# Kernel tuning notes

Hardware: AMD Instinct MI355X
Metric: run time of the kernel (lower is better)

The kernel has to match this reference:

```python
import jax, jax.numpy as jnp
import numpy as np

NUM_CLASSES = 81
OUTPUT_SIZE = 19
NMS_THRESH = 0.45
TOP_K = 400          # pre-NMS candidates per class == max_output_size of tf NMS
KEEP_TOP_K = 200
CONF_THRESH = 0.01
MASK_CONF_THRESH = 0.6
B = 8
P = 24564


def setup_inputs() -> dict:
    key = jax.random.key(0)
    k1, k2, k3, k4 = jax.random.split(key, 4)
    # structured x = [loc | conf | priorbox | variances] so the decode math is realistic
    loc = 0.1 * jax.random.normal(k1, (B, P, 4), dtype=jnp.float32)
    conf = jax.random.uniform(k2, (B, P, NUM_CLASSES), dtype=jnp.float32)
    cxcy = jax.random.uniform(k3, (P, 2), minval=0.05, maxval=0.95)
    wh = jax.random.uniform(k4, (P, 2), minval=0.05, maxval=0.3)
    pmin = jnp.clip(cxcy - 0.5 * wh, 0.0, 1.0)
    pmax = jnp.clip(cxcy + 0.5 * wh, 0.0, 1.0)
    priors = jnp.broadcast_to(jnp.concatenate([pmin, pmax], -1), (B, P, 4)).astype(jnp.float32)
    variances = jnp.full((B, P, 4), 0.1, dtype=jnp.float32)
    x = jnp.concatenate([loc, conf, priors, variances], -1)
    return {"x": x}


def decode_boxes(loc, prior, var):
    pw = prior[..., 2] - prior[..., 0]
    ph = prior[..., 3] - prior[..., 1]
    pcx = 0.5 * (prior[..., 2] + prior[..., 0])
    pcy = 0.5 * (prior[..., 3] + prior[..., 1])
    cx = loc[..., 0] * pw * var[..., 0] + pcx
    cy = loc[..., 1] * pw * var[..., 1] + pcy  # uses prior_width, faithful to original code
    w = jnp.exp(loc[..., 2] * var[..., 2]) * pw
    h = jnp.exp(loc[..., 3] * var[..., 3]) * ph
    box = jnp.stack([cx - 0.5 * w, cy - 0.5 * h, cx + 0.5 * w, cy + 0.5 * h], -1)
    return jnp.clip(box, 0.0, 1.0)


def iou_matrix(b):  # [N,4] xyxy -> [N,N]
    area = (b[:, 2] - b[:, 0]) * (b[:, 3] - b[:, 1])
    ix1 = jnp.maximum(b[:, None, 0], b[None, :, 0])
    iy1 = jnp.maximum(b[:, None, 1], b[None, :, 1])
    ix2 = jnp.minimum(b[:, None, 2], b[None, :, 2])
    iy2 = jnp.minimum(b[:, None, 3], b[None, :, 3])
    inter = jnp.maximum(ix2 - ix1, 0.0) * jnp.maximum(iy2 - iy1, 0.0)
    union = area[:, None] + area[None, :] - inter
    return jnp.where(union > 0.0, inter / union, 0.0)


def greedy_nms(iou, valid):  # candidates already sorted desc by score
    n = valid.shape[0]
    def body(kept, i):
        sup = jnp.any(kept & (iou[i] > NMS_THRESH))
        return kept.at[i].set(valid[i] & ~sup), None
    kept, _ = jax.lax.scan(body, jnp.zeros(n, dtype=bool), jnp.arange(n))
    return kept


def _forward(x):
    b = x.shape[0]
    loc = x[..., :4]
    conf = x[..., 4:4 + NUM_CLASSES]
    prior = x[..., -8:-4]
    var = x[..., -4:]
    boxes = decode_boxes(loc, prior, var)                        # [B,P,4]
    cls_conf = jnp.swapaxes(conf[..., 1:], 1, 2)                 # [B,C-1,P] (skip background class 0)
    masked = jnp.where(cls_conf > CONF_THRESH, cls_conf, -1.0)
    scores, idx = jax.lax.top_k(masked, TOP_K)                   # [B,C-1,K]
    cand = jnp.take_along_axis(boxes[:, None], idx[..., None], axis=2)  # [B,C-1,K,4]
    valid = scores > CONF_THRESH
    iou = jax.vmap(jax.vmap(iou_matrix))(cand)                   # [B,C-1,K,K]
    kept = jax.vmap(jax.vmap(greedy_nms))(iou, valid)            # [B,C-1,K]
    labels = jnp.broadcast_to(jnp.arange(1, NUM_CLASSES)[None, :, None], scores.shape)
    det_scores = jnp.where(kept, scores, -1.0).reshape(b, -1)
    det_boxes = cand.reshape(b, -1, 4)
    det_labels = labels.reshape(b, -1)
    order = jnp.argsort(-det_scores, axis=1)[:, :KEEP_TOP_K]     # sort desc by conf, keep_top_k=200
    top_s = jnp.take_along_axis(det_scores, order, 1)            # [B,200]
    top_b = jnp.take_along_axis(det_boxes, order[..., None], 1)  # [B,200,4]
    top_l = jnp.take_along_axis(det_labels, order, 1)            # [B,200]

    def rasterize(s, bx, lb):
        vld = s >= MASK_CONF_THRESH
        co = jnp.round(bx * OUTPUT_SIZE).astype(jnp.int32)       # [K,4] x1,y1,x2,y2
        g = jnp.arange(OUTPUT_SIZE)
        cover = ((g[None, :, None] >= co[:, 1, None, None]) & (g[None, :, None] < co[:, 3, None, None]) &
                 (g[None, None, :] >= co[:, 0, None, None]) & (g[None, None, :] < co[:, 2, None, None]) &
                 vld[:, None, None])                             # [K,S,S]
        chan = lb - 1                                            # label-1 channel, as in original
        kidx = jnp.arange(KEEP_TOP_K)
        def per_channel(c):
            cov = cover & (chan == c)[:, None, None]
            win = jnp.max(jnp.where(cov, kidx[:, None, None], -1), axis=0)  # [S,S]
            return jnp.where(win >= 0, s[jnp.clip(win, 0)], 0.0)
        return jnp.transpose(jax.vmap(per_channel)(jnp.arange(NUM_CLASSES)), (1, 2, 0))

    return jax.vmap(rasterize)(top_s, top_b, top_l)              # [B,S,S,C]


def reference(x):
    return _forward(x)
```

## Files before the change

### kernel.cpp

```cpp
#include <hip/hip_runtime.h>

#define NB 8
#define NP 24564
#define NCLS 80
#define TOPK 400
#define KEEPK 200
#define OUTS 19
#define NCELL (OUTS * OUTS)
#define DETN (NCLS * TOPK)
#define CKS 32008
#define ROWS 128
#define CHUNKS ((NP + ROWS - 1) / ROWS)
#define CAP 1024
#define T0 0.972f
#define NT 512
#define LCAP 24
#define CSTR 16
#define SUBS 8
#define SUBCAP 128
#define WTASK 2704
#define TILN 676
#define SKW(i) ((unsigned)(i) + ((unsigned)(i) >> 5))
#define SELN (TOPK + (TOPK >> 5) + 4)

__device__ __forceinline__ unsigned f2ord(float f) {
    unsigned u = __float_as_uint(f);
    return (u & 0x80000000u) ? ~u : (u | 0x80000000u);
}
__device__ __forceinline__ float ord2f(unsigned k) {
    unsigned u = (k & 0x80000000u) ? (k & 0x7fffffffu) : ~k;
    return __uint_as_float(u);
}
__device__ __forceinline__ unsigned bin16(unsigned key) {
    int b = (int)(key >> 16) - 0xBC00;
    b = b < 0 ? 0 : (b > 1023 ? 1023 : b);
    return (unsigned)b;
}

__device__ __forceinline__ unsigned long long shfl_xor_u64(unsigned long long v, int mask) {
    unsigned lo = (unsigned)__shfl_xor((int)(unsigned)v, mask);
    unsigned hi = (unsigned)__shfl_xor((int)(v >> 32), mask);
    return ((unsigned long long)hi << 32) | lo;
}

__device__ __forceinline__ void regsort1024(unsigned long long& a0, unsigned long long& a1,
                                            unsigned long long* sc, unsigned t) {
    const unsigned e0 = 2u * t;
#pragma unroll
    for (unsigned k = 2; k <= 1024; k <<= 1) {
#pragma unroll
        for (unsigned j = k >> 1; j >= 128; j >>= 1) {
            sc[e0] = a0; sc[e0 + 1] = a1;
            __syncthreads();
            unsigned p0 = e0 ^ j;
            unsigned long long b0 = sc[p0], b1 = sc[p0 + 1];
            bool km = ((e0 & k) == 0u) ^ ((e0 & j) != 0u);
            a0 = km ? (a0 > b0 ? a0 : b0) : (a0 < b0 ? a0 : b0);
            a1 = km ? (a1 > b1 ? a1 : b1) : (a1 < b1 ? a1 : b1);
            __syncthreads();
        }
#pragma unroll
        for (unsigned j = ((k >> 1) < 64u ? (k >> 1) : 64u); j >= 2; j >>= 1) {
            unsigned long long b0 = shfl_xor_u64(a0, (int)(j >> 1));
            unsigned long long b1 = shfl_xor_u64(a1, (int)(j >> 1));
            bool km = ((e0 & k) == 0u) ^ ((e0 & j) != 0u);
            a0 = km ? (a0 > b0 ? a0 : b0) : (a0 < b0 ? a0 : b0);
            a1 = km ? (a1 > b1 ? a1 : b1) : (a1 < b1 ? a1 : b1);
        }
        {
            bool dir = ((e0 & k) == 0u);
            unsigned long long mx = a0 > a1 ? a0 : a1;
            unsigned long long mn = a0 > a1 ? a1 : a0;
            a0 = dir ? mx : mn;
            a1 = dir ? mn : mx;
        }
    }
}

__device__ __forceinline__ void bitonic_desc(unsigned long long* cand, unsigned S, int tid) {
    for (unsigned k = 2; k <= S; k <<= 1)
        for (unsigned j = k >> 1; j; j >>= 1) {
            for (unsigned i = tid; i < S; i += NT) {
                unsigned l = i ^ j;
                if (l > i) {
                    unsigned long long a = cand[i], bq = cand[l];
                    bool sw = ((i & k) == 0) ? (a < bq) : (a > bq);
                    if (sw) { cand[i] = bq; cand[l] = a; }
                }
            }
            __syncthreads();
        }
}

__global__ __launch_bounds__(256) void kZ(unsigned* __restrict__ ccnt,
                                          unsigned* __restrict__ gflag,
                                          unsigned* __restrict__ kcnt) {
    int t = blockIdx.x * 256 + threadIdx.x;
    for (int i = t; i < NB * NCLS * SUBS * CSTR; i += gridDim.x * 256) ccnt[i] = 0u;
    if (t < NB * NCLS) gflag[t] = 0u;
    if (t < NB * 16) kcnt[t] = 0u;
}

__global__ __launch_bounds__(NT) void kA(const float* __restrict__ x,
                                         float4* __restrict__ boxes,
                                         unsigned long long* __restrict__ pcand,
                                         unsigned* __restrict__ ccnt,
                                         unsigned* __restrict__ gflag) {
    __shared__ float tile[ROWS * 93];
    __shared__ unsigned long long list[NCLS * LCAP];
    __shared__ unsigned lcnt[NCLS];
    __shared__ unsigned lbase[NCLS];

    int blk = blockIdx.x;
    int b = blk / CHUNKS, chunk = blk % CHUNKS;
    unsigned sub = (unsigned)(chunk & (SUBS - 1));
    int p0 = chunk * ROWS;
    int nrows = NP - p0; if (nrows > ROWS) nrows = ROWS;
    const float* src = x + (size_t)(b * NP + p0) * 93;
    int total4 = (nrows * 93) >> 2;
    const float4* s4 = (const float4*)src;
    float4* t4 = (float4*)tile;
    for (int e = threadIdx.x; e < total4; e += NT) t4[e] = s4[e];
    __syncthreads();

    int lane = threadIdx.x & 63;
    int cg = threadIdx.x >> 6;
    for (int c = cg; c < NCLS; c += (NT / 64)) {
        unsigned cnt = 0u;
        for (int h = 0; h < 2; ++h) {
            int row = h * 64 + lane;
            float v = (row < nrows) ? tile[row * 93 + 5 + c] : -1.0f;
            bool pred = v > T0;
            unsigned long long bal = __ballot(pred);
            if (pred) {
                unsigned r = cnt + (unsigned)__popcll(bal & ((1ull << lane) - 1ull));
                if (r < LCAP)
                    list[c * LCAP + r] =
                        ((unsigned long long)f2ord(v) << 32) |
                        (unsigned)(~(unsigned)(p0 + row));
            }
            cnt += (unsigned)__popcll(bal);
        }
        if (lane == 0) lcnt[c] = cnt;
    }
    __syncthreads();

    if (threadIdx.x >= 128 && threadIdx.x < 128 + NCLS) {
        int c = threadIdx.x - 128;
        unsigned n = lcnt[c];
        unsigned wr = (n > LCAP) ? LCAP : n;
        unsigned old = 0u;
        if (wr) old = atomicAdd(&ccnt[((b * NCLS + c) * SUBS + sub) * CSTR], wr);
        lbase[c] = old;
        lcnt[c] = wr;
        if (n > LCAP || old + wr > SUBCAP) gflag[b * NCLS + c] = 1u;
    }
    if (threadIdx.x < nrows) {
        const float* r = tile + threadIdx.x * 93;
        float l0 = r[0], l1 = r[1], l2 = r[2], l3 = r[3];
        float px1 = r[85], py1 = r[86], px2 = r[87], py2 = r[88];
        float v0 = r[89], v1 = r[90], v2 = r[91], v3 = r[92];
        float pw = px2 - px1, ph = py2 - py1;
        float pcx = 0.5f * (px2 + px1), pcy = 0.5f * (py2 + py1);
        float cx = l0 * pw * v0 + pcx;
        float cy = l1 * pw * v1 + pcy;
        float w = expf(l2 * v2) * pw;
        float h = expf(l3 * v3) * ph;
        float x1 = fminf(fmaxf(cx - 0.5f * w, 0.f), 1.f);
        float y1 = fminf(fmaxf(cy - 0.5f * h, 0.f), 1.f);
        float x2 = fminf(fmaxf(cx + 0.5f * w, 0.f), 1.f);
        float y2 = fminf(fmaxf(cy + 0.5f * h, 0.f), 1.f);
        boxes[(size_t)b * NP + p0 + threadIdx.x] = make_float4(x1, y1, x2, y2);
    }
    __syncthreads();

    for (int idx = threadIdx.x; idx < NCLS * LCAP; idx += NT) {
        int c = idx / LCAP, i = idx - c * LCAP;
        if ((unsigned)i < lcnt[c]) {
            unsigned pos = lbase[c] + (unsigned)i;
            if (pos < SUBCAP)
                pcand[((size_t)(b * NCLS + c) << 10) + sub * SUBCAP + pos] = list[idx];
        }
    }
}

__device__ void select_strided(const float* __restrict__ src, unsigned needed,
                               unsigned long long* cand,
                               unsigned* hist, unsigned* aux, unsigned* scal,
                               int tid) {
    for (int i = tid; i < 1024; i += NT) hist[i] = 0u;
    if (tid == 0) { scal[0] = 0u; scal[1] = 0u; scal[2] = 0u; scal[3] = 0u; }
    __syncthreads();
    for (int p = tid; p < NP; p += NT) {
        float v = src[(size_t)p * 93];
        float m = (v > 0.01f) ? v : -1.0f;
        atomicAdd(&hist[bin16(f2ord(m))], 1u);
    }
    __syncthreads();
    unsigned h0 = 0, h1 = 0, h2 = 0, h3 = 0;
    if (tid < 256) {
        h0 = hist[4 * tid]; h1 = hist[4 * tid + 1];
        h2 = hist[4 * tid + 2]; h3 = hist[4 * tid + 3];
        aux[tid] = h0 + h1 + h2 + h3;
    }
    __syncthreads();
    for (int d = 1; d < 256; d <<= 1) {
        unsigned v = 0u;
        if (tid < 256 && tid + d < 256) v = aux[tid + d];
        __syncthreads();
        if (tid < 256) aux[tid] += v;
        __syncthreads();
    }
    if (tid < 256) {
        unsigned above = (tid < 255) ? aux[tid + 1] : 0u;
        unsigned s3 = above + h3, s2 = s3 + h2, s1 = s2 + h1, s0 = s1 + h0;
        if (s0 >= needed && s1 < needed) { scal[0] = 4 * tid;     scal[1] = s1;    scal[2] = s0; }
        if (s1 >= needed && s2 < needed) { scal[0] = 4 * tid + 1; scal[1] = s2;    scal[2] = s1; }
        if (s2 >= needed && s3 < needed) { scal[0] = 4 * tid + 2; scal[1] = s3;    scal[2] = s2; }
        if (s3 >= needed && above < needed) { scal[0] = 4 * tid + 3; scal[1] = above; scal[2] = s3; }
    }
    __syncthreads();
    unsigned cb = scal[0], countHigh = scal[1], countAt = scal[2];
    unsigned cut8 = 0;
    if (countAt > CAP) {
        if (tid < 256) aux[tid] = 0u;
        __syncthreads();
        for (int p = tid; p < NP; p += NT) {
            float v = src[(size_t)p * 93];
            float m = (v > 0.01f) ? v : -1.0f;
            unsigned k = f2ord(m);
            if (bin16(k) == cb) atomicAdd(&aux[(k >> 8) & 255u], 1u);
        }
        __syncthreads();
        for (int d = 1; d < 256; d <<= 1) {
            unsigned v = 0u;
            if (tid < 256 && tid + d < 256) v = aux[tid + d];
            __syncthreads();
            if (tid < 256) aux[tid] += v;
            __syncthreads();
        }
        if (tid < 256) {
            unsigned suf8 = aux[tid];
            unsigned sufN = (tid < 255) ? aux[tid + 1] : 0u;
            unsigned need2 = needed - countHigh;
            if (suf8 >= need2 && sufN < need2) scal[3] = (unsigned)tid;
        }
        __syncthreads();
        cut8 = scal[3];
    }
    __syncthreads();
    if (tid == 0) scal[1] = 0u;
    __syncthreads();
    for (int p = tid; p < NP; p += NT) {
        float v = src[(size_t)p * 93];
        float m = (v > 0.01f) ? v : -1.0f;
        unsigned key = f2ord(m);
        unsigned b16 = bin16(key);
        bool take = (b16 > cb) || (b16 == cb && ((key >> 8) & 255u) >= cut8);
        if (take) {
            unsigned pos = atomicAdd(&scal[1], 1u);
            if (pos < CAP) cand[pos] = ((unsigned long long)key << 32) | (unsigned)(~p);
        }
    }
    __syncthreads();
    unsigned cc = scal[1]; if (cc > CAP) cc = CAP;
    for (unsigned i = tid; i < CAP; i += NT) if (i >= cc) cand[i] = 0ull;
    __syncthreads();
    bitonic_desc(cand, (cc <= 512u) ? 512u : (unsigned)CAP, tid);
}

union ScratchU {
    unsigned long long sc[1024];
    unsigned iouRowP[WTASK];
    struct { unsigned long long cand[CAP]; unsigned hist[1024]; unsigned aux[256]; } fb;
};

__global__ __launch_bounds__(NT) void kNms(const float* __restrict__ x,
                                           const float4* __restrict__ boxes,
                                           const unsigned long long* __restrict__ pcand,
                                           const unsigned* __restrict__ ccnt,
                                           const unsigned* __restrict__ gflag,
                                           unsigned long long* __restrict__ ckeys,
                                           float4* __restrict__ cboxesC,
                                           unsigned* __restrict__ kcnt) {
    __shared__ ScratchU U;
    __shared__ float4 selBox[SELN];
    __shared__ float selArea[SELN];
    __shared__ unsigned selKey[SELN];
    __shared__ unsigned short taskGW[TILN];
    __shared__ unsigned csub[SUBS];
    __shared__ unsigned scal[4];
    __shared__ unsigned Vsh;
    __shared__ unsigned keptWords[13];

    int b = blockIdx.x / NCLS, c = blockIdx.x % NCLS;
    int tid = threadIdx.x;
    unsigned t = (unsigned)tid;

    if (tid == 0) Vsh = 0u;
    if (tid < 100) {
        unsigned g = t, v = g >> 3, r = g & 7u;
        unsigned O = g + 4u * v * (v - 1u) + r * v;
        for (unsigned w = 0; w <= v; ++w)
            taskGW[O + w] = (unsigned short)((g << 4) | w);
    }
    if (tid < SUBS) {
        unsigned v = ccnt[((b * NCLS + c) * SUBS + t) * CSTR];
        csub[t] = (v > SUBCAP) ? (unsigned)SUBCAP : v;
    }
    unsigned gf = gflag[b * NCLS + c];
    __syncthreads();
    unsigned total = csub[0] + csub[1] + csub[2] + csub[3]
                   + csub[4] + csub[5] + csub[6] + csub[7];

    bool fast = (gf == 0u) && (total >= TOPK);
    unsigned long long a0, a1;
    if (fast) {
        const ulonglong2* src2 =
            (const ulonglong2*)(pcand + ((size_t)(b * NCLS + c) << 10));
        ulonglong2 vv = src2[t];
        unsigned s = t >> 6;
        unsigned o0 = (2u * t) & (SUBCAP - 1u);
        unsigned cs = csub[s];
        a0 = (o0     < cs) ? vv.x : 0ull;
        a1 = (o0 + 1 < cs) ? vv.y : 0ull;
        regsort1024(a0, a1, U.sc, t);
    } else {
        select_strided(x + (size_t)b * NP * 93 + 5 + c, TOPK,
                       U.fb.cand, U.fb.hist, U.fb.aux, scal, tid);
        a0 = U.fb.cand[2u * t];
        a1 = U.fb.cand[2u * t + 1];
    }
    const unsigned VALID_KEY = f2ord(0.01f);
    if (t < TOPK / 2) {
        unsigned i0 = ~(unsigned)a0; if (i0 >= NP) i0 = 0;
        unsigned i1 = ~(unsigned)a1; if (i1 >= NP) i1 = 0;
        float4 b0 = boxes[(size_t)b * NP + i0];
        float4 b1 = boxes[(size_t)b * NP + i1];
        selBox[SKW(2u * t)] = b0;            selBox[SKW(2u * t + 1)] = b1;
        selArea[SKW(2u * t)] = (b0.z - b0.x) * (b0.w - b0.y);
        selArea[SKW(2u * t + 1)] = (b1.z - b1.x) * (b1.w - b1.y);
        selKey[SKW(2u * t)] = (unsigned)(a0 >> 32);
        selKey[SKW(2u * t + 1)] = (unsigned)(a1 >> 32);
    }
    {
        bool v0 = (t < TOPK / 2) && ((unsigned)(a0 >> 32) > VALID_KEY);
        bool v1 = (t < TOPK / 2) && ((unsigned)(a1 >> 32) > VALID_KEY);
        unsigned long long bv0 = __ballot(v0), bv1 = __ballot(v1);
        if ((t & 63u) == 0u)
            atomicAdd(&Vsh, (unsigned)(__popcll(bv0) + __popcll(bv1)));
    }
    __syncthreads();

    for (int T = tid; T < TILN; T += NT) {
        unsigned gw = (unsigned)taskGW[T];
        unsigned g = gw >> 4, w = gw & 15u;
        unsigned r0 = 4u * g;
        float4 br0 = selBox[SKW(r0)];     float ar0 = selArea[SKW(r0)];
        float4 br1 = selBox[SKW(r0 + 1)]; float ar1 = selArea[SKW(r0 + 1)];
        float4 br2 = selBox[SKW(r0 + 2)]; float ar2 = selArea[SKW(r0 + 2)];
        float4 br3 = selBox[SKW(r0 + 3)]; float ar3 = selArea[SKW(r0 + 3)];
        unsigned w0 = 0, w1 = 0, w2 = 0, w3 = 0;
#pragma unroll 8
        for (int jj = 0; jj < 32; ++jj) {
            int j = (int)(w * 32u) + jj;
            float4 bj = selBox[SKW(j)];
            float aj = selArea[SKW(j)];
#define IOU1(BR, AR, WRD) { \
            float ix = fminf(BR.z, bj.z) - fmaxf(BR.x, bj.x); \
            float iy = fminf(BR.w, bj.w) - fmaxf(BR.y, bj.y); \
            float inter = fmaxf(ix, 0.f) * fmaxf(iy, 0.f); \
            float uni = AR + aj - inter; \
            WRD |= (unsigned)(inter > 0.45f * uni) << jj; }
            IOU1(br0, ar0, w0) IOU1(br1, ar1, w1)
            IOU1(br2, ar2, w2) IOU1(br3, ar3, w3)
#undef IOU1
        }
        unsigned band = g >> 3;
        unsigned baseo = (band + 1u) * (16u * band + (r0 & 31u)) + w;
        U.iouRowP[baseo]                   = w0;
        U.iouRowP[baseo +      (band + 1u)] = w1;
        U.iouRowP[baseo + 2u * (band + 1u)] = w2;
        U.iouRowP[baseo + 3u * (band + 1u)] = w3;
    }
    __syncthreads();

    if (tid < 64) {
        unsigned lane = t;
        unsigned myKept = 0;
        unsigned V = Vsh;
        unsigned q0 = U.iouRowP[0 + lane], q1 = U.iouRowP[1 + lane];
        unsigned q2 = U.iouRowP[2 + lane], q3 = U.iouRowP[3 + lane];
        unsigned q4 = U.iouRowP[4 + lane], q5 = U.iouRowP[5 + lane];
        unsigned q6 = U.iouRowP[6 + lane], q7 = U.iouRowP[7 + lane];
#define STEP(Q, II) { \
        unsigned w_ = Q; \
        int ip_ = (II) + 8; \
        if (ip_ < TOPK) { \
            unsigned bb_ = (unsigned)ip_ >> 5; \
            Q = U.iouRowP[(bb_ + 1u) * (16u * bb_ + ((unsigned)ip_ & 31u)) + lane]; \
        } \
        bool hit_ = (w_ & myKept) != 0u; \
        unsigned long long bal_ = __ballot(hit_); \
        if ((unsigned)(II) < V && bal_ == 0ull && lane == ((unsigned)(II) >> 5)) \
            myKept |= 1u << ((II) & 31); }
        for (int i = 0; i < TOPK; i += 8) {
            STEP(q0, i)     STEP(q1, i + 1) STEP(q2, i + 2) STEP(q3, i + 3)
            STEP(q4, i + 4) STEP(q5, i + 5) STEP(q6, i + 6) STEP(q7, i + 7)
        }
#undef STEP
        if (lane < 13) keptWords[lane] = myKept;
    }
    __syncthreads();

    if (tid == 0) {
        unsigned total2 = 0;
        for (int w = 0; w < 13; ++w) total2 += __popc(keptWords[w]);
        scal[2] = atomicAdd(&kcnt[b * 16], total2);
    }
    __syncthreads();
    unsigned base = scal[2];
    size_t kb = (size_t)b * CKS;
    for (int k = tid; k < TOPK; k += NT) {
        bool kept = (keptWords[k >> 5] >> (k & 31)) & 1u;
        if (kept) {
            unsigned rank = 0;
            int wi = k >> 5;
            for (int w = 0; w < wi; ++w) rank += __popc(keptWords[w]);
            rank += __popc(keptWords[wi] & ((1u << (k & 31)) - 1u));
            unsigned idx = base + rank;
            ckeys[kb + idx] =
                ((unsigned long long)selKey[SKW(k)] << 32) |
                (unsigned)(~(((unsigned)c << 16) | idx));
            cboxesC[kb + idx] = selBox[SKW(k)];
        }
    }
}

struct HistU { unsigned hist[1024]; unsigned aux[256]; };

__global__ __launch_bounds__(NT) void kC(const unsigned long long* __restrict__ ckeys,
                                         const float4* __restrict__ cboxesC,
                                         const unsigned* __restrict__ kcnt,
                                         float* __restrict__ out) {
    __shared__ unsigned long long cand[CAP];
    __shared__ unsigned long long scK[CAP];
    __shared__ HistU S;
    __shared__ unsigned scal[4];
    __shared__ float eS[KEEPK];
    __shared__ int eC0[KEEPK], eC1[KEEPK], eC2[KEEPK], eC3[KEEPK];
    __shared__ int eCh[KEEPK];

    int b = blockIdx.x;
    int tid = threadIdx.x;
    unsigned t = (unsigned)tid;
    const ulonglong2* k2 = (const ulonglong2*)(ckeys + (size_t)b * CKS);
    int n = (int)kcnt[b * 16]; if (n > DETN) n = DETN;
    int n2 = (n + 1) >> 1;
    const unsigned needed = KEEPK;

    for (int i = tid; i < 1024; i += NT) S.hist[i] = 0u;
    if (tid == 0) { scal[0] = 0u; scal[1] = 0u; scal[2] = 0u; scal[3] = 0u; }
    __syncthreads();
    for (int i = tid; i < n2; i += NT) {
        ulonglong2 v = k2[i];
        atomicAdd(&S.hist[bin16((unsigned)(v.x >> 32))], 1u);
        if (2 * i + 1 < n) atomicAdd(&S.hist[bin16((unsigned)(v.y >> 32))], 1u);
    }
    __syncthreads();
    unsigned h0 = 0, h1 = 0, h2 = 0, h3 = 0;
    if (tid < 256) {
        h0 = S.hist[4 * tid]; h1 = S.hist[4 * tid + 1];
        h2 = S.hist[4 * tid + 2]; h3 = S.hist[4 * tid + 3];
        S.aux[tid] = h0 + h1 + h2 + h3;
    }
    __syncthreads();
    for (int d = 1; d < 256; d <<= 1) {
        unsigned v = 0u;
        if (tid < 256 && tid + d < 256) v = S.aux[tid + d];
        __syncthreads();
        if (tid < 256) S.aux[tid] += v;
        __syncthreads();
    }
    if (tid < 256) {
        unsigned above = (tid < 255) ? S.aux[tid + 1] : 0u;
        unsigned s3 = above + h3, s2 = s3 + h2, s1 = s2 + h1, s0 = s1 + h0;
        if (s0 >= needed && s1 < needed) { scal[0] = 4 * tid;     scal[1] = s1;    scal[2] = s0; }
        if (s1 >= needed && s2 < needed) { scal[0] = 4 * tid + 1; scal[1] = s2;    scal[2] = s1; }
        if (s2 >= needed && s3 < needed) { scal[0] = 4 * tid + 2; scal[1] = s3;    scal[2] = s2; }
        if (s3 >= needed && above < needed) { scal[0] = 4 * tid + 3; scal[1] = above; scal[2] = s3; }
    }
    __syncthreads();
    unsigned cb = scal[0], countHigh = scal[1], countAt = scal[2];
    unsigned cut8 = 0;
    if (countAt > CAP) {
        if (tid < 256) S.aux[tid] = 0u;
        __syncthreads();
        for (int i = tid; i < n2; i += NT) {
            ulonglong2 v = k2[i];
            unsigned kx = (unsigned)(v.x >> 32), ky = (unsigned)(v.y >> 32);
            if (bin16(kx) == cb) atomicAdd(&S.aux[(kx >> 8) & 255u], 1u);
            if (2 * i + 1 < n && bin16(ky) == cb) atomicAdd(&S.aux[(ky >> 8) & 255u], 1u);
        }
        __syncthreads();
        for (int d = 1; d < 256; d <<= 1) {
            unsigned v = 0u;
            if (tid < 256 && tid + d < 256) v = S.aux[tid + d];
            __syncthreads();
            if (tid < 256) S.aux[tid] += v;
            __syncthreads();
        }
        if (tid < 256) {
            unsigned suf8 = S.aux[tid];
            unsigned sufN = (tid < 255) ? S.aux[tid + 1] : 0u;
            unsigned need2 = needed - countHigh;
            if (suf8 >= need2 && sufN < need2) scal[3] = (unsigned)tid;
        }
        __syncthreads();
        cut8 = scal[3];
    }
    __syncthreads();
    if (tid == 0) scal[1] = 0u;
    __syncthreads();
    for (int i = tid; i < n2; i += NT) {
        ulonglong2 v = k2[i];
#pragma unroll
        for (int c = 0; c < 2; ++c) {
            if (c && 2 * i + 1 >= n) continue;
            unsigned long long key = c ? v.y : v.x;
            unsigned kh = (unsigned)(key >> 32);
            unsigned b16 = bin16(kh);
            bool take = (b16 > cb) || (b16 == cb && ((kh >> 8) & 255u) >= cut8);
            if (take) {
                unsigned pos = atomicAdd(&scal[1], 1u);
                if (pos < CAP) cand[pos] = key;
            }
        }
    }
    __syncthreads();
    unsigned cc = scal[1]; if (cc > CAP) cc = CAP;
    for (unsigned i = tid; i < CAP; i += NT) if (i >= cc) cand[i] = 0ull;
    __syncthreads();
    unsigned long long a0 = cand[2u * t], a1 = cand[2u * t + 1];
    __syncthreads();
    regsort1024(a0, a1, scK, t);

    if (t < KEEPK / 2) {
#pragma unroll
        for (int q = 0; q < 2; ++q) {
            unsigned long long K = q ? a1 : a0;
            unsigned k = 2u * t + q;
            unsigned key = (unsigned)(K >> 32);
            unsigned lo = ~(unsigned)K;
            unsigned ch = lo >> 16;
            unsigned idx = lo & 0xffffu;
            if (ch >= NCLS) { ch = 0; idx = 0; }
            float4 bx = cboxesC[(size_t)b * CKS + idx];
            eS[k] = (key == 0u) ? -1.0f : ord2f(key);
            eC0[k] = (int)rintf(bx.x * (float)OUTS);
            eC1[k] = (int)rintf(bx.y * (float)OUTS);
            eC2[k] = (int)rintf(bx.z * (float)OUTS);
            eC3[k] = (int)rintf(bx.w * (float)OUTS);
            eCh[k] = (int)ch;
        }
    }
    __syncthreads();

    for (int cell = tid; cell < NCELL; cell += NT) {
        int y = cell / OUTS, x = cell % OUTS;
        float* o = out + ((size_t)b * NCELL + cell) * 81;
        for (int ch = 0; ch < 81; ++ch) o[ch] = 0.f;
        for (int k = 0; k < KEEPK; ++k) {
            float s = eS[k];
            if (s < 0.6f) continue;
            if (y >= eC1[k] && y < eC3[k] && x >= eC0[k] && x < eC2[k])
                o[eCh[k]] = s;
        }
    }
}

extern "C" void kernel_launch(void* const* d_in, const int* in_sizes, int n_in,
                              void* d_out, int out_size, void* d_ws, size_t ws_size,
                              hipStream_t stream) {
    const float* x = (const float*)d_in[0];
    float* out = (float*)d_out;

    float4* boxes   = (float4*)d_ws;
    float4* cboxesC = boxes + (size_t)NB * NP;
    unsigned long long* ckeys = (unsigned long long*)(cboxesC + (size_t)NB * CKS);
    unsigned long long* pcand = ckeys + (size_t)NB * CKS;
    unsigned* ccnt = (unsigned*)(pcand + ((size_t)NB * NCLS << 10));
    unsigned* gflag = ccnt + NB * NCLS * SUBS * CSTR;
    unsigned* kcnt  = gflag + NB * NCLS;

    kZ<<<40, 256, 0, stream>>>(ccnt, gflag, kcnt);
    kA<<<NB * CHUNKS, NT, 0, stream>>>(x, boxes, pcand, ccnt, gflag);
    kNms<<<NB * NCLS, NT, 0, stream>>>(x, boxes, pcand, ccnt, gflag, ckeys, cboxesC, kcnt);
    kC<<<NB, NT, 0, stream>>>(ckeys, cboxesC, kcnt, out);
}
```

Baseline: 237.4 us.

## Bucket candidates by score range so per-class top-k needs only wave-local sorts

```diff
diff --git a/kernel.cpp b/kernel.cpp
--- a/kernel.cpp
+++ b/kernel.cpp
@@ -36,11 +36,38 @@
     b = b < 0 ? 0 : (b > 1023 ? 1023 : b);
     return (unsigned)b;
 }
+__device__ __forceinline__ int sbucket(float v) {
+    int bkt = (int)((v - T0) * 285.7142f);
+    return bkt < 0 ? 0 : (bkt > 7 ? 7 : bkt);
+}
 
 __device__ __forceinline__ unsigned long long shfl_xor_u64(unsigned long long v, int mask) {
     unsigned lo = (unsigned)__shfl_xor((int)(unsigned)v, mask);
     unsigned hi = (unsigned)__shfl_xor((int)(v >> 32), mask);
     return ((unsigned long long)hi << 32) | lo;
+}
+
+__device__ __forceinline__ void wave_sort128(unsigned long long& a0, unsigned long long& a1,
+                                             unsigned lane) {
+    const unsigned e0 = 2u * lane;
+#pragma unroll
+    for (unsigned k = 2; k <= 128; k <<= 1) {
+#pragma unroll
+        for (unsigned j = k >> 1; j >= 2; j >>= 1) {
+            unsigned long long b0 = shfl_xor_u64(a0, (int)(j >> 1));
+            unsigned long long b1 = shfl_xor_u64(a1, (int)(j >> 1));
+            bool km = ((e0 & k) == 0u) ^ ((e0 & j) != 0u);
+            a0 = km ? (a0 > b0 ? a0 : b0) : (a0 < b0 ? a0 : b0);
+            a1 = km ? (a1 > b1 ? a1 : b1) : (a1 < b1 ? a1 : b1);
+        }
+        {
+            bool dir = ((e0 & k) == 0u);
+            unsigned long long mx = a0 > a1 ? a0 : a1;
+            unsigned long long mn = a0 > a1 ? a1 : a0;
+            a0 = dir ? mx : mn;
+            a1 = dir ? mn : mx;
+        }
+    }
 }
 
 __device__ __forceinline__ void regsort1024(unsigned long long& a0, unsigned long long& a1,
@@ -109,11 +136,11 @@
     __shared__ float tile[ROWS * 93];
     __shared__ unsigned long long list[NCLS * LCAP];
     __shared__ unsigned lcnt[NCLS];
-    __shared__ unsigned lbase[NCLS];
+    __shared__ unsigned lbaseB[NCLS * SUBS];
+    __shared__ unsigned short posArr[NCLS * LCAP];
 
     int blk = blockIdx.x;
     int b = blk / CHUNKS, chunk = blk % CHUNKS;
-    unsigned sub = (unsigned)(chunk & (SUBS - 1));
     int p0 = chunk * ROWS;
     int nrows = NP - p0; if (nrows > ROWS) nrows = ROWS;
     const float* src = x + (size_t)(b * NP + p0) * 93;
@@ -149,11 +176,40 @@
         int c = threadIdx.x - 128;
         unsigned n = lcnt[c];
         unsigned wr = (n > LCAP) ? LCAP : n;
-        unsigned old = 0u;
-        if (wr) old = atomicAdd(&ccnt[((b * NCLS + c) * SUBS + sub) * CSTR], wr);
-        lbase[c] = old;
-        lcnt[c] = wr;
-        if (n > LCAP || old + wr > SUBCAP) gflag[b * NCLS + c] = 1u;
+        unsigned n0 = 0, n1 = 0, n2 = 0, n3 = 0, n4 = 0, n5 = 0, n6 = 0, n7 = 0;
+        for (unsigned i = 0; i < wr; ++i) {
+            unsigned key = (unsigned)(list[c * LCAP + i] >> 32);
+            int bkt = sbucket(ord2f(key));
+            unsigned r;
+            if      (bkt == 0) r = n0++;
+            else if (bkt == 1) r = n1++;
+            else if (bkt == 2) r = n2++;
+            else if (bkt == 3) r = n3++;
+            else if (bkt == 4) r = n4++;
+            else if (bkt == 5) r = n5++;
+            else if (bkt == 6) r = n6++;
+            else               r = n7++;
+            posArr[c * LCAP + i] = (unsigned short)((unsigned)bkt * SUBCAP + r);
+        }
+        unsigned* cp = &ccnt[(b * NCLS + c) * SUBS * CSTR];
+        unsigned o0 = 0, o1 = 0, o2 = 0, o3 = 0, o4 = 0, o5 = 0, o6 = 0, o7 = 0;
+        if (n0) o0 = atomicAdd(cp + 0 * CSTR, n0);
+        if (n1) o1 = atomicAdd(cp + 1 * CSTR, n1);
+        if (n2) o2 = atomicAdd(cp + 2 * CSTR, n2);
+        if (n3) o3 = atomicAdd(cp + 3 * CSTR, n3);
+        if (n4) o4 = atomicAdd(cp + 4 * CSTR, n4);
+        if (n5) o5 = atomicAdd(cp + 5 * CSTR, n5);
+        if (n6) o6 = atomicAdd(cp + 6 * CSTR, n6);
+        if (n7) o7 = atomicAdd(cp + 7 * CSTR, n7);
+        unsigned ovf = (unsigned)(n > LCAP);
+        ovf |= (o0 + n0 > SUBCAP) | (o1 + n1 > SUBCAP) | (o2 + n2 > SUBCAP)
+             | (o3 + n3 > SUBCAP) | (o4 + n4 > SUBCAP) | (o5 + n5 > SUBCAP)
+             | (o6 + n6 > SUBCAP) | (o7 + n7 > SUBCAP);
+        if (ovf) gflag[b * NCLS + c] = 1u;
+        lbaseB[c * SUBS + 0] = o0; lbaseB[c * SUBS + 1] = o1;
+        lbaseB[c * SUBS + 2] = o2; lbaseB[c * SUBS + 3] = o3;
+        lbaseB[c * SUBS + 4] = o4; lbaseB[c * SUBS + 5] = o5;
+        lbaseB[c * SUBS + 6] = o6; lbaseB[c * SUBS + 7] = o7;
     }
     if (threadIdx.x < nrows) {
         const float* r = tile + threadIdx.x * 93;
@@ -176,10 +232,13 @@
 
     for (int idx = threadIdx.x; idx < NCLS * LCAP; idx += NT) {
         int c = idx / LCAP, i = idx - c * LCAP;
-        if ((unsigned)i < lcnt[c]) {
-            unsigned pos = lbase[c] + (unsigned)i;
+        unsigned n = lcnt[c]; if (n > LCAP) n = LCAP;
+        if ((unsigned)i < n) {
+            unsigned pr = (unsigned)posArr[idx];
+            unsigned bkt = pr >> 7;
+            unsigned pos = lbaseB[c * SUBS + bkt] + (pr & 127u);
             if (pos < SUBCAP)
-                pcand[((size_t)(b * NCLS + c) << 10) + sub * SUBCAP + pos] = list[idx];
+                pcand[((size_t)(b * NCLS + c) << 10) + bkt * SUBCAP + pos] = list[idx];
         }
     }
 }
@@ -314,36 +373,53 @@
                    + csub[4] + csub[5] + csub[6] + csub[7];
 
     bool fast = (gf == 0u) && (total >= TOPK);
-    unsigned long long a0, a1;
     if (fast) {
         const ulonglong2* src2 =
             (const ulonglong2*)(pcand + ((size_t)(b * NCLS + c) << 10));
         ulonglong2 vv = src2[t];
         unsigned s = t >> 6;
-        unsigned o0 = (2u * t) & (SUBCAP - 1u);
+        unsigned lane = t & 63u;
+        unsigned e0 = 2u * lane;
         unsigned cs = csub[s];
-        a0 = (o0     < cs) ? vv.x : 0ull;
-        a1 = (o0 + 1 < cs) ? vv.y : 0ull;
-        regsort1024(a0, a1, U.sc, t);
+        unsigned long long a0 = (e0     < cs) ? vv.x : 0ull;
+        unsigned long long a1 = (e0 + 1 < cs) ? vv.y : 0ull;
+        wave_sort128(a0, a1, lane);
+        unsigned off = 0;
+#pragma unroll
+        for (unsigned b2 = 0; b2 < SUBS; ++b2) if (b2 > s) off += csub[b2];
+        unsigned r0 = off + e0, r1 = off + e0 + 1u;
+        if (e0 < cs && r0 < TOPK) {
+            unsigned i0 = ~(unsigned)a0; if (i0 >= NP) i0 = 0;
+            float4 bx = boxes[(size_t)b * NP + i0];
+            selBox[SKW(r0)] = bx;
+            selArea[SKW(r0)] = (bx.z - bx.x) * (bx.w - bx.y);
+            selKey[SKW(r0)] = (unsigned)(a0 >> 32);
+        }
+        if (e0 + 1 < cs && r1 < TOPK) {
+            unsigned i1 = ~(unsigned)a1; if (i1 >= NP) i1 = 0;
+            float4 bx = boxes[(size_t)b * NP + i1];
+            selBox[SKW(r1)] = bx;
+            selArea[SKW(r1)] = (bx.z - bx.x) * (bx.w - bx.y);
+            selKey[SKW(r1)] = (unsigned)(a1 >> 32);
+        }
+        if (tid == 0) Vsh = TOPK;
     } else {
         select_strided(x + (size_t)b * NP * 93 + 5 + c, TOPK,
                        U.fb.cand, U.fb.hist, U.fb.aux, scal, tid);
-        a0 = U.fb.cand[2u * t];
-        a1 = U.fb.cand[2u * t + 1];
-    }
-    const unsigned VALID_KEY = f2ord(0.01f);
-    if (t < TOPK / 2) {
-        unsigned i0 = ~(unsigned)a0; if (i0 >= NP) i0 = 0;
-        unsigned i1 = ~(unsigned)a1; if (i1 >= NP) i1 = 0;
-        float4 b0 = boxes[(size_t)b * NP + i0];
-        float4 b1 = boxes[(size_t)b * NP + i1];
-        selBox[SKW(2u * t)] = b0;            selBox[SKW(2u * t + 1)] = b1;
-        selArea[SKW(2u * t)] = (b0.z - b0.x) * (b0.w - b0.y);
-        selArea[SKW(2u * t + 1)] = (b1.z - b1.x) * (b1.w - b1.y);
-        selKey[SKW(2u * t)] = (unsigned)(a0 >> 32);
-        selKey[SKW(2u * t + 1)] = (unsigned)(a1 >> 32);
-    }
-    {
+        unsigned long long a0 = U.fb.cand[2u * t];
+        unsigned long long a1 = U.fb.cand[2u * t + 1];
+        const unsigned VALID_KEY = f2ord(0.01f);
+        if (t < TOPK / 2) {
+            unsigned i0 = ~(unsigned)a0; if (i0 >= NP) i0 = 0;
+            unsigned i1 = ~(unsigned)a1; if (i1 >= NP) i1 = 0;
+            float4 b0 = boxes[(size_t)b * NP + i0];
+            float4 b1 = boxes[(size_t)b * NP + i1];
+            selBox[SKW(2u * t)] = b0;            selBox[SKW(2u * t + 1)] = b1;
+            selArea[SKW(2u * t)] = (b0.z - b0.x) * (b0.w - b0.y);
+            selArea[SKW(2u * t + 1)] = (b1.z - b1.x) * (b1.w - b1.y);
+            selKey[SKW(2u * t)] = (unsigned)(a0 >> 32);
+            selKey[SKW(2u * t + 1)] = (unsigned)(a1 >> 32);
+        }
         bool v0 = (t < TOPK / 2) && ((unsigned)(a0 >> 32) > VALID_KEY);
         bool v1 = (t < TOPK / 2) && ((unsigned)(a1 >> 32) > VALID_KEY);
         unsigned long long bv0 = __ballot(v0), bv1 = __ballot(v1);
```

Result: slower. 245.2 us (+3.3%).
